# Performance work log

Hardware: AMD Instinct MI355X
Metric: run time of the kernel (lower is better)

The kernel has to match this reference:

```python
import jax, jax.numpy as jnp
import numpy as np

B = 1_000_000

def _lin(key, out_f, in_f):
    k1, k2 = jax.random.split(key)
    lim = 1.0 / np.sqrt(in_f)
    W = jax.random.uniform(k1, (out_f, in_f), jnp.float32, -lim, lim)
    b = jax.random.uniform(k2, (out_f,), jnp.float32, -lim, lim)
    return W, b

def setup_inputs() -> dict:
    key = jax.random.key(0)
    ks = jax.random.split(key, 10)
    x = jax.random.normal(ks[0], (B, 73), dtype=jnp.float32)
    a = jax.random.randint(ks[1], (B,), 0, 1000).astype(jnp.float32)
    b = jax.random.randint(ks[2], (B,), 0, 10000).astype(jnp.float32)
    x = x.at[:, 0].set(a).at[:, 1].set(b)
    W1, b1 = _lin(ks[3], 64, 73)
    W2, b2 = _lin(ks[4], 32, 64)
    Wres, bres = _lin(ks[5], 32, 32)
    W6, b6 = _lin(ks[6], 1, 32)
    return {
        'x': x,
        'alpha': 0.1 * jax.random.normal(ks[7], (1000,), jnp.float32),
        'beta': 0.1 * jax.random.normal(ks[8], (10000,), jnp.float32),
        'gamma': 0.1 * jax.random.normal(ks[9], (24,), jnp.float32),
        'g': jnp.float32(1.0),
        'W1': W1, 'b1': b1, 'W2': W2, 'b2': b2,
        'Wres': Wres, 'bres': bres, 'W6': W6, 'b6': b6,
    }

def reference(x, alpha, beta, gamma, g, W1, b1, W2, b2, Wres, bres, W6, b6):
    # gather-based feature embed for columns 0 and 1
    a = x[:, 0].astype(jnp.int32)
    b = x[:, 1].astype(jnp.int32)
    x = x.at[:, 0].set(alpha[a]).at[:, 1].set(beta[b])
    # per-column scale for columns 3..22 (fused as one slice multiply)
    x = x.at[:, 3:23].multiply(gamma[3:23])
    h = jax.nn.gelu(x @ W1.T + b1, approximate=False)   # [B,64]
    h = jax.nn.gelu(h @ W2.T + b2, approximate=False)   # [B,32]
    # dropout in eval mode == identity
    h = jax.nn.gelu(h @ Wres.T + bres + h, approximate=False)  # residual [B,32]
    return h @ W6.T + b6 + g                             # [B,1]
```

## Files before the change

### kernel.cpp

```cpp
#include <hip/hip_runtime.h>
#include <math.h>

typedef _Float16 half8 __attribute__((ext_vector_type(8)));
typedef __fp16   fp16x2 __attribute__((ext_vector_type(2)));
typedef float f32x4 __attribute__((ext_vector_type(4)));

__device__ __forceinline__ float gelu_f(float v) {
    float y  = v * 0.70710678118654752f;
    float ay = __builtin_fabsf(y);
    float t  = __builtin_amdgcn_rcpf(__builtin_fmaf(0.3275911f, ay, 1.0f));
    float p  = __builtin_fmaf(t, 1.061405429f, -1.453152027f);
    p = __builtin_fmaf(p, t, 1.421413741f);
    p = __builtin_fmaf(p, t, -0.284496736f);
    p = __builtin_fmaf(p, t, 0.254829592f);
    p = p * t;
    float e  = __builtin_amdgcn_exp2f(ay * ay * -1.4426950408889634f);
    float er = __builtin_fmaf(-p, e, 1.0f);
    er = __builtin_copysignf(er, v);
    float hv = 0.5f * v;
    return __builtin_fmaf(hv, er, hv);
}

#define MFMA16(A, B, C) __builtin_amdgcn_mfma_f32_16x16x32_f16((A), (B), (C), 0, 0, 0)

__global__ __launch_bounds__(512, 4) void mlp_mfma_kernel(
    const float* __restrict__ x,
    const float* __restrict__ alpha,
    const float* __restrict__ beta,
    const float* __restrict__ gamma,
    const float* __restrict__ gscal,
    const float* __restrict__ W1, const float* __restrict__ b1,
    const float* __restrict__ W2, const float* __restrict__ b2,
    const float* __restrict__ Wres, const float* __restrict__ bres,
    const float* __restrict__ W6, const float* __restrict__ b6,
    float* __restrict__ out, int B)
{
    const int lane = threadIdx.x & 63;
    const int wid  = threadIdx.x >> 6;
    const int c    = lane & 15;
    const int g    = lane >> 4;

    __shared__ __align__(16) _Float16 wtab[18 * 512];
    __shared__ __align__(16) _Float16 h1buf[8][16 * 72];
    __shared__ __align__(16) _Float16 h2buf[8][16 * 40];
    _Float16* __restrict__ h1b = h1buf[wid];
    _Float16* __restrict__ h2b = h2buf[wid];

    if (wid == 0) {
        float gm[8];
        #pragma unroll
        for (int j = 0; j < 8; ++j) {
            int k  = 8 * g + j;
            int kc = k < 3 ? 3 : (k > 22 ? 22 : k);
            float gv = gamma[kc];
            gm[j] = (k >= 3 && k < 23) ? gv : 1.0f;
        }
        #pragma unroll
        for (int t = 0; t < 4; ++t)
            #pragma unroll
            for (int s = 0; s < 3; ++s)
                #pragma unroll
                for (int j = 0; j < 8; ++j) {
                    int k  = 32 * s + 8 * g + j;
                    int kc = k < 73 ? k : 72;
                    float v = W1[(16 * t + c) * 73 + kc];
                    if (s == 0) v *= gm[j];
                    wtab[(t * 3 + s) * 512 + lane * 8 + j] =
                        (k < 73) ? (_Float16)v : (_Float16)0.f;
                }
        #pragma unroll
        for (int t = 0; t < 2; ++t)
            #pragma unroll
            for (int s = 0; s < 2; ++s)
                #pragma unroll
                for (int j = 0; j < 8; ++j)
                    wtab[(12 + t * 2 + s) * 512 + lane * 8 + j] =
                        (_Float16)W2[(16 * t + c) * 64 + 32 * s + 8 * g + j];
        #pragma unroll
        for (int t = 0; t < 2; ++t)
            #pragma unroll
            for (int j = 0; j < 8; ++j)
                wtab[(16 + t) * 512 + lane * 8 + j] =
                    (_Float16)Wres[(16 * t + c) * 32 + 8 * g + j];
    }

    float b1f[4], b2f[2], brf[2], w6f[2];
    #pragma unroll
    for (int t = 0; t < 4; ++t) b1f[t] = b1[16 * t + c];
    #pragma unroll
    for (int t = 0; t < 2; ++t) { b2f[t] = b2[16 * t + c]; brf[t] = bres[16 * t + c]; w6f[t] = W6[16 * t + c]; }
    const float b6g = b6[0] + gscal[0];

    __syncthreads();

    const _Float16* wt = wtab + lane * 8;

    const int ntiles = B >> 4;
    const int totw   = gridDim.x * 8;
    for (int tile = blockIdx.x * 8 + wid; tile < ntiles; tile += totw) {
        const int R0 = tile << 4;
        const float* __restrict__ xr = x + (size_t)(R0 + c) * 73;

        float xv0[8], xv1[8], xv2[8];
        #pragma unroll
        for (int j = 0; j < 8; ++j) xv0[j] = xr[8 * g + j];
        #pragma unroll
        for (int j = 0; j < 8; ++j) xv1[j] = xr[32 + 8 * g + j];
        #pragma unroll
        for (int j = 0; j < 8; ++j) {
            int k = 64 + 8 * g + j;
            float v = xr[k < 73 ? k : 72];
            xv2[j] = (k < 73) ? v : 0.f;
        }

        float xa = 0.f, xb = 0.f;
        if (g == 0) {
            xa = alpha[(int)xv0[0]];
            xb = beta[(int)xv0[1]];
        }

        half8 w1f[4][3];
        #pragma unroll
        for (int t = 0; t < 4; ++t)
            #pragma unroll
            for (int s = 0; s < 3; ++s)
                w1f[t][s] = *reinterpret_cast<const half8*>(wt + (t * 3 + s) * 512);

        union H8 { half8 h8; fp16x2 h2[4]; };
        H8 a1u, a2u;
        #pragma unroll
        for (int j = 0; j < 4; ++j) {
            a1u.h2[j] = __builtin_amdgcn_cvt_pkrtz(xv1[2 * j], xv1[2 * j + 1]);
            a2u.h2[j] = __builtin_amdgcn_cvt_pkrtz(xv2[2 * j], xv2[2 * j + 1]);
        }
        f32x4 acc[4];
        #pragma unroll
        for (int t = 0; t < 4; ++t) { f32x4 z = { b1f[t], b1f[t], b1f[t], b1f[t] }; acc[t] = z; }
        #pragma unroll
        for (int t = 0; t < 4; ++t) acc[t] = MFMA16(a1u.h8, w1f[t][1], acc[t]);
        #pragma unroll
        for (int t = 0; t < 4; ++t) acc[t] = MFMA16(a2u.h8, w1f[t][2], acc[t]);

        H8 a0u;
        #pragma unroll
        for (int j = 0; j < 4; ++j)
            a0u.h2[j] = __builtin_amdgcn_cvt_pkrtz(xv0[2 * j], xv0[2 * j + 1]);
        {
            fp16x2 we = __builtin_amdgcn_cvt_pkrtz(xa, xb);
            if (g == 0) a0u.h2[0] = we;
        }
        #pragma unroll
        for (int t = 0; t < 4; ++t) acc[t] = MFMA16(a0u.h8, w1f[t][0], acc[t]);

        #pragma unroll
        for (int t = 0; t < 4; ++t)
            #pragma unroll
            for (int r = 0; r < 4; ++r)
                h1b[(4 * g + r) * 72 + 16 * t + c] = (_Float16)gelu_f(acc[t][r]);

        asm volatile("s_waitcnt lgkmcnt(0)" ::: "memory");

        half8 w2f[2][2];
        #pragma unroll
        for (int t = 0; t < 2; ++t)
            #pragma unroll
            for (int s = 0; s < 2; ++s)
                w2f[t][s] = *reinterpret_cast<const half8*>(wt + (12 + t * 2 + s) * 512);

        half8 a2f0 = *reinterpret_cast<const half8*>(&h1b[c * 72 + 8 * g]);
        half8 a2f1 = *reinterpret_cast<const half8*>(&h1b[c * 72 + 32 + 8 * g]);
        f32x4 ac2[2];
        #pragma unroll
        for (int t = 0; t < 2; ++t) {
            f32x4 z = { b2f[t], b2f[t], b2f[t], b2f[t] };
            z = MFMA16(a2f0, w2f[t][0], z);
            ac2[t] = MFMA16(a2f1, w2f[t][1], z);
        }
        float h2c[2][4];
        #pragma unroll
        for (int t = 0; t < 2; ++t)
            #pragma unroll
            for (int r = 0; r < 4; ++r)
                h2c[t][r] = gelu_f(ac2[t][r]);

        #pragma unroll
        for (int t = 0; t < 2; ++t)
            #pragma unroll
            for (int r = 0; r < 4; ++r)
                h2b[(4 * g + r) * 40 + 16 * t + c] = (_Float16)h2c[t][r];

        asm volatile("s_waitcnt lgkmcnt(0)" ::: "memory");

        half8 wrf[2];
        #pragma unroll
        for (int t = 0; t < 2; ++t)
            wrf[t] = *reinterpret_cast<const half8*>(wt + (16 + t) * 512);

        half8 arf = *reinterpret_cast<const half8*>(&h2b[c * 40 + 8 * g]);
        f32x4 acr[2];
        #pragma unroll
        for (int t = 0; t < 2; ++t) {
            f32x4 z = { brf[t] + h2c[t][0], brf[t] + h2c[t][1],
                        brf[t] + h2c[t][2], brf[t] + h2c[t][3] };
            acr[t] = MFMA16(arf, wrf[t], z);
        }

        f32x4 p;
        #pragma unroll
        for (int r = 0; r < 4; ++r)
            p[r] = gelu_f(acr[0][r]) * w6f[0] + gelu_f(acr[1][r]) * w6f[1];
        #pragma unroll
        for (int m = 1; m < 16; m <<= 1) {
            #pragma unroll
            for (int r = 0; r < 4; ++r) p[r] += __shfl_xor(p[r], m, 64);
        }
        if (c == 0) {
            f32x4 o = { p[0] + b6g, p[1] + b6g, p[2] + b6g, p[3] + b6g };
            *reinterpret_cast<f32x4*>(out + R0 + 4 * g) = o;
        }
    }
}

extern "C" void kernel_launch(void* const* d_in, const int* in_sizes, int n_in,
                              void* d_out, int out_size, void* d_ws, size_t ws_size,
                              hipStream_t stream) {
    const float* x     = (const float*)d_in[0];
    const float* alpha = (const float*)d_in[1];
    const float* beta  = (const float*)d_in[2];
    const float* gamma = (const float*)d_in[3];
    const float* g     = (const float*)d_in[4];
    const float* W1    = (const float*)d_in[5];
    const float* b1    = (const float*)d_in[6];
    const float* W2    = (const float*)d_in[7];
    const float* b2    = (const float*)d_in[8];
    const float* Wres  = (const float*)d_in[9];
    const float* bres  = (const float*)d_in[10];
    const float* W6    = (const float*)d_in[11];
    const float* b6    = (const float*)d_in[12];
    float* out = (float*)d_out;

    int B = out_size;
    int nblocks = 768;
    mlp_mfma_kernel<<<nblocks, 512, 0, stream>>>(x, alpha, beta, gamma, g,
                                                 W1, b1, W2, b2, Wres, bres,
                                                 W6, b6, out, B);
}
```

Before: 96.77 us.

## Prefetch next x tile into LDS via global_load_lds double-issue pipeline

Each wave now stages its 16-row x tile into a per-wave LDS buffer using direct global-to-LDS loads, and issues the next tile's load as soon as the current tile's values are read into registers. Global reads become contiguous 16-byte transfers instead of strided per-row scalar loads, and load latency is meant to overlap with the MFMA/GELU compute. The h2 buffer is aliased onto h1buf to save LDS, and the grid is reduced from 768 to 512 blocks, which matches the larger LDS footprint cutting occupancy. Risks: a single staging buffer reused without double-buffering relies on waitcnt ordering, and the larger LDS use may lower waves per CU.

After: 97.09 us. No clear change (+0.3%).

```diff
diff --git a/kernel.cpp b/kernel.cpp
--- a/kernel.cpp
+++ b/kernel.cpp
@@ -22,6 +22,11 @@
 }
 
 #define MFMA16(A, B, C) __builtin_amdgcn_mfma_f32_16x16x32_f16((A), (B), (C), 0, 0, 0)
+
+#define GLOAD_LDS16(gsrc, ldst)                                              \
+    __builtin_amdgcn_global_load_lds(                                        \
+        (const __attribute__((address_space(1))) void*)(gsrc),               \
+        (__attribute__((address_space(3))) void*)(ldst), 16, 0, 0)
 
 __global__ __launch_bounds__(512, 4) void mlp_mfma_kernel(
     const float* __restrict__ x,
@@ -41,10 +46,10 @@
     const int g    = lane >> 4;
 
     __shared__ __align__(16) _Float16 wtab[18 * 512];
+    __shared__ __align__(16) float xstage[8][16 * 73];
     __shared__ __align__(16) _Float16 h1buf[8][16 * 72];
-    __shared__ __align__(16) _Float16 h2buf[8][16 * 40];
-    _Float16* __restrict__ h1b = h1buf[wid];
-    _Float16* __restrict__ h2b = h2buf[wid];
+    float*     xs  = xstage[wid];
+    _Float16*  h1b = h1buf[wid];
 
     if (wid == 0) {
         float gm[8];
@@ -97,19 +102,34 @@
 
     const int ntiles = B >> 4;
     const int totw   = gridDim.x * 8;
-    for (int tile = blockIdx.x * 8 + wid; tile < ntiles; tile += totw) {
+    const int tile0  = blockIdx.x * 8 + wid;
+
+    {
+        const char* src = (const char*)(x + (size_t)(tile0 << 4) * 73);
+        char* dst = (char*)xs;
+        #pragma unroll
+        for (int q = 0; q < 4; ++q)
+            GLOAD_LDS16(src + q * 1024 + lane * 16, dst + q * 1024);
+        if (lane < 36)
+            GLOAD_LDS16(src + 4096 + lane * 16, dst + 4096);
+    }
+
+    for (int tile = tile0; tile < ntiles; tile += totw) {
         const int R0 = tile << 4;
-        const float* __restrict__ xr = x + (size_t)(R0 + c) * 73;
-
+
+        asm volatile("s_waitcnt vmcnt(0)" ::: "memory");
+
+        const float* xrow = xs + c * 73;
         float xv0[8], xv1[8], xv2[8];
         #pragma unroll
-        for (int j = 0; j < 8; ++j) xv0[j] = xr[8 * g + j];
-        #pragma unroll
-        for (int j = 0; j < 8; ++j) xv1[j] = xr[32 + 8 * g + j];
+        for (int j = 0; j < 8; ++j) xv0[j] = xrow[8 * g + j];
+        #pragma unroll
+        for (int j = 0; j < 8; ++j) xv1[j] = xrow[32 + 8 * g + j];
         #pragma unroll
         for (int j = 0; j < 8; ++j) {
-            int k = 64 + 8 * g + j;
-            float v = xr[k < 73 ? k : 72];
+            int k  = 64 + 8 * g + j;
+            int kc = k < 73 ? k : 72;
+            float v = xrow[kc];
             xv2[j] = (k < 73) ? v : 0.f;
         }
 
@@ -117,6 +137,20 @@
         if (g == 0) {
             xa = alpha[(int)xv0[0]];
             xb = beta[(int)xv0[1]];
+        }
+
+        asm volatile("s_waitcnt lgkmcnt(0)" ::: "memory");
+        {
+            const int nt = tile + totw;
+            if (nt < ntiles) {
+                const char* src = (const char*)(x + (size_t)(nt << 4) * 73);
+                char* dst = (char*)xs;
+                #pragma unroll
+                for (int q = 0; q < 4; ++q)
+                    GLOAD_LDS16(src + q * 1024 + lane * 16, dst + q * 1024);
+                if (lane < 36)
+                    GLOAD_LDS16(src + 4096 + lane * 16, dst + 4096);
+            }
         }
 
         half8 w1f[4][3];
@@ -187,7 +221,7 @@
         for (int t = 0; t < 2; ++t)
             #pragma unroll
             for (int r = 0; r < 4; ++r)
-                h2b[(4 * g + r) * 40 + 16 * t + c] = (_Float16)h2c[t][r];
+                h1b[(4 * g + r) * 40 + 16 * t + c] = (_Float16)h2c[t][r];
 
         asm volatile("s_waitcnt lgkmcnt(0)" ::: "memory");
 
@@ -196,7 +230,7 @@
         for (int t = 0; t < 2; ++t)
             wrf[t] = *reinterpret_cast<const half8*>(wt + (16 + t) * 512);
 
-        half8 arf = *reinterpret_cast<const half8*>(&h2b[c * 40 + 8 * g]);
+        half8 arf = *reinterpret_cast<const half8*>(&h1b[c * 40 + 8 * g]);
         f32x4 acr[2];
         #pragma unroll
         for (int t = 0; t < 2; ++t) {
@@ -240,7 +274,7 @@
     float* out = (float*)d_out;
 
     int B = out_size;
-    int nblocks = 768;
+    int nblocks = 512;
     mlp_mfma_kernel<<<nblocks, 512, 0, stream>>>(x, alpha, beta, gamma, g,
                                                  W1, b1, W2, b2, Wres, bres,
                                                  W6, b6, out, B);
```
